# Kernel optimization log

Hardware: AMD Instinct MI355X
Metric: run time of the kernel (lower is better)

Reference implementation:

```python
import jax, jax.numpy as jnp
import numpy as np

B, S, D_IN, D_OUT = 4, 2048, 1024, 64
USE_MASK = True

def setup_inputs() -> dict:
    key = jax.random.key(0)
    ks = jax.random.split(key, 6)
    return {
        "inputs_for_keys": jax.random.normal(ks[0], (B, S, D_IN), jnp.float32),
        "inputs_for_values": jax.random.normal(ks[1], (B, S, D_IN), jnp.float32),
        "inputs_for_queries": jax.random.normal(ks[2], (B, S, D_IN), jnp.float32),
        "Weight_Q": jax.random.normal(ks[3], (D_IN, D_OUT), jnp.float32) * 0.02,
        "Weight_K": jax.random.normal(ks[4], (D_IN, D_OUT), jnp.float32) * 0.02,
        "Weight_V": jax.random.normal(ks[5], (D_IN, D_OUT), jnp.float32) * 0.02,
    }

def reference(inputs_for_keys, inputs_for_values, inputs_for_queries, Weight_Q, Weight_K, Weight_V):
    Q = jnp.einsum('bsd,de->bse', inputs_for_queries, Weight_Q)
    K = jnp.einsum('bsd,de->bse', inputs_for_keys, Weight_K)
    V = jnp.einsum('bsd,de->bse', inputs_for_values, Weight_V)
    # scores: [B, S_q, S_k], scaled by sqrt(d_out)
    scores = jnp.einsum('bqe,bke->bqk', Q, K) / np.sqrt(D_OUT).astype(np.float32)
    if USE_MASK:
        # -inf strictly above the diagonal (causal mask), matching
        # transpose(tril(ones*-inf, -1)) in the original.
        q_idx = jnp.arange(S)[:, None]
        k_idx = jnp.arange(S)[None, :]
        scores = jnp.where(k_idx > q_idx, -jnp.inf, scores)
    attn = jax.nn.softmax(scores, axis=-1)
    return jnp.einsum('bqk,bke->bqe', attn, V)
```

## Files before the change

### kernel.cpp

```cpp
#include <hip/hip_runtime.h>
#include <hip/hip_bf16.h>
#include <stdint.h>

typedef __bf16 bf16_t;
typedef __bf16 bf16x8 __attribute__((ext_vector_type(8)));
typedef float f32x4 __attribute__((ext_vector_type(4)));

#define L2E 1.44269504088896340736f

static __device__ __forceinline__ f32x4 mfma16(bf16x8 a, bf16x8 b, f32x4 c) {
  return __builtin_amdgcn_mfma_f32_16x16x32_bf16(a, b, c, 0, 0, 0);
}

static __device__ __forceinline__ void gload_lds16(const void* g, void* l) {
  __builtin_amdgcn_global_load_lds(
      (const __attribute__((address_space(1))) uint32_t*)g,
      (__attribute__((address_space(3))) uint32_t*)l, 16, 0, 0);
}

__global__ __launch_bounds__(256) void wt_kernel(const float* __restrict__ Wq,
                                                 const float* __restrict__ Wk,
                                                 const float* __restrict__ Wv,
                                                 bf16_t* __restrict__ Wt) {
  int gid = blockIdx.x * 256 + threadIdx.x;
  int proj = gid >> 16;
  int rem = gid & 65535;
  int k = rem >> 6, n = rem & 63;
  const float* W = (proj == 0) ? Wq : (proj == 1) ? Wk : Wv;
  float v = W[rem];
  if (proj == 0) v *= 0.125f;
  Wt[proj * 65536 + n * 1024 + k] = (bf16_t)v;
}

__global__ __launch_bounds__(384, 1) void proj_kernel(
    const float* __restrict__ Xq, const float* __restrict__ Xk, const float* __restrict__ Xv,
    const bf16_t* __restrict__ Wt,
    bf16_t* __restrict__ Qb, bf16_t* __restrict__ Kb, bf16_t* __restrict__ Vt) {
  __shared__ alignas(16) char Wl[131072];
  __shared__ alignas(16) bf16_t Osm[6][16][72];

  int tid = threadIdx.x;
  int w = tid / 64, lane = tid & 63;
  int l15 = lane & 15, g = lane >> 4;
  int bid = blockIdx.x;

  int p_lds = (bid * 6 + 2) >> 9;

  {
    const char* wb = (const char*)(Wt + (size_t)p_lds * 65536);
    for (int n = w; n < 64; n += 6) {
#pragma unroll
      for (int h = 0; h < 2; ++h) {
        const char* src = wb + n * 2048 + h * 1024 + ((lane * 16) ^ ((n & 7) << 4));
        gload_lds16(src, Wl + n * 2048 + h * 1024);
      }
    }
  }
  __syncthreads();

  int T = bid * 6 + w;
  int p = T >> 9;
  int t = T & 511;
  int m0 = t * 16;
  const float* X = (p == 0) ? Xq : (p == 1) ? Xk : Xv;
  const float* xrow = X + (size_t)(m0 + l15) * 1024 + g * 8;

  f32x4 acc[4] = {};

  auto wfrag_lds = [&](int ct, int byteoff) -> bf16x8 {
    int n = ct * 16 + l15;
    return *(const bf16x8*)(Wl + n * 2048 + (byteoff ^ ((n & 7) << 4)));
  };
  auto wfrag_glob = [&](int ct, int byteoff) -> bf16x8 {
    int n = ct * 16 + l15;
    return *(const bf16x8*)((const char*)(Wt + (size_t)p * 65536) + n * 2048 + byteoff);
  };

  auto run = [&](auto wf) {
    float4 pa[2][4];
    auto ld = [&](int j, float4* r) {
      const float* b = xrow + j * 64;
      r[0] = *(const float4*)b;        r[1] = *(const float4*)(b + 4);
      r[2] = *(const float4*)(b + 32); r[3] = *(const float4*)(b + 36);
    };
    ld(0, pa[0]);
#pragma unroll
    for (int j = 0; j < 16; ++j) {
      if (j < 15) ld(j + 1, pa[(j + 1) & 1]);
      float4* r = pa[j & 1];
      bf16x8 a0, a1;
      a0[0] = (bf16_t)r[0].x; a0[1] = (bf16_t)r[0].y; a0[2] = (bf16_t)r[0].z; a0[3] = (bf16_t)r[0].w;
      a0[4] = (bf16_t)r[1].x; a0[5] = (bf16_t)r[1].y; a0[6] = (bf16_t)r[1].z; a0[7] = (bf16_t)r[1].w;
      a1[0] = (bf16_t)r[2].x; a1[1] = (bf16_t)r[2].y; a1[2] = (bf16_t)r[2].z; a1[3] = (bf16_t)r[2].w;
      a1[4] = (bf16_t)r[3].x; a1[5] = (bf16_t)r[3].y; a1[6] = (bf16_t)r[3].z; a1[7] = (bf16_t)r[3].w;
#pragma unroll
      for (int ct = 0; ct < 4; ++ct) {
        acc[ct] = mfma16(a0, wf(ct, j * 128 + g * 16), acc[ct]);
        acc[ct] = mfma16(a1, wf(ct, j * 128 + 64 + g * 16), acc[ct]);
      }
    }
  };
  if (p == p_lds) run(wfrag_lds); else run(wfrag_glob);

#pragma unroll
  for (int ct = 0; ct < 4; ++ct)
#pragma unroll
    for (int r = 0; r < 4; ++r)
      Osm[w][g * 4 + r][ct * 16 + l15] = (bf16_t)acc[ct][r];

  if (p < 2) {
    bf16_t* Ob = (p == 0) ? Qb : Kb;
    int row = lane >> 2, c0 = (lane & 3) * 16;
    uint4 v0 = *(const uint4*)&Osm[w][row][c0];
    uint4 v1 = *(const uint4*)&Osm[w][row][c0 + 8];
    *(uint4*)&Ob[(size_t)(m0 + row) * 64 + c0] = v0;
    *(uint4*)&Ob[(size_t)(m0 + row) * 64 + c0 + 8] = v1;
  } else {
    int d = lane;
    bf16_t tmp[16];
#pragma unroll
    for (int s = 0; s < 16; ++s) tmp[s] = Osm[w][s][d];
    int b = t >> 7, s0 = (t & 127) * 16;
    bf16_t* dst = Vt + ((size_t)(b * 64 + d)) * 2048 + s0;
    *(uint4*)dst = *(const uint4*)&tmp[0];
    *(uint4*)(dst + 8) = *(const uint4*)&tmp[8];
  }
}

#define NW 8
__global__ __launch_bounds__(512) void attn_kernel(
    const bf16_t* __restrict__ Qb, const bf16_t* __restrict__ Kb,
    const bf16_t* __restrict__ Vt, float* __restrict__ Out) {
  __shared__ alignas(16) char Psm[NW * 4096];
  __shared__ float accL[NW][32][64];
  __shared__ float mL[NW][32];
  __shared__ float lL[NW][32];

  int b = blockIdx.y;
  int x = blockIdx.x;
  int qt = (b >= 2) ? (63 - x) : x;
  int q0 = qt * 32;
  int tid = threadIdx.x;
  int w = tid >> 6, lane = tid & 63;
  int l15 = lane & 15, g = lane >> 4;
  char* Pw = Psm + w * 4096;

  bf16x8 qf[2][2];
#pragma unroll
  for (int h = 0; h < 2; ++h) {
    size_t qrow = (size_t)(b * 2048 + q0 + h * 16 + l15) * 64;
    qf[h][0] = *(const bf16x8*)(Qb + qrow + g * 8);
    qf[h][1] = *(const bf16x8*)(Qb + qrow + 32 + g * 8);
  }

  float m_run[2][4], l_run[2][4];
  f32x4 acc_o[2][4] = {};
#pragma unroll
  for (int h = 0; h < 2; ++h)
#pragma unroll
    for (int r = 0; r < 4; ++r) { m_run[h][r] = -1e30f; l_run[h][r] = 0.f; }

  int ntiles = (q0 + 95) >> 6;
  const bf16_t* kbase = Kb + (size_t)b * 2048 * 64;
  const bf16_t* vbase = Vt + (size_t)b * 64 * 2048;

  for (int t = w; t < ntiles; t += NW) {
    int kv0 = t * 64;
    f32x4 s[2][4] = {};
#pragma unroll
    for (int ct = 0; ct < 4; ++ct) {
      const bf16_t* kr = kbase + (size_t)(kv0 + ct * 16 + l15) * 64 + g * 8;
      bf16x8 kf0 = *(const bf16x8*)kr;
      bf16x8 kf1 = *(const bf16x8*)(kr + 32);
#pragma unroll
      for (int h = 0; h < 2; ++h) {
        s[h][ct] = mfma16(qf[h][0], kf0, s[h][ct]);
        s[h][ct] = mfma16(qf[h][1], kf1, s[h][ct]);
      }
    }
    if (t == ntiles - 1) {
#pragma unroll
      for (int h = 0; h < 2; ++h)
#pragma unroll
        for (int ct = 0; ct < 4; ++ct)
#pragma unroll
          for (int r = 0; r < 4; ++r) {
            int kg_ = kv0 + ct * 16 + l15;
            int qg_ = q0 + h * 16 + g * 4 + r;
            if (kg_ > qg_) s[h][ct][r] = -1e30f;
          }
    }

#pragma unroll
    for (int h = 0; h < 2; ++h)
#pragma unroll
      for (int r = 0; r < 4; ++r) {
        float mx = fmaxf(fmaxf(s[h][0][r], s[h][1][r]), fmaxf(s[h][2][r], s[h][3][r]));
        mx = fmaxf(mx, __shfl_xor(mx, 1, 64));
        mx = fmaxf(mx, __shfl_xor(mx, 2, 64));
        mx = fmaxf(mx, __shfl_xor(mx, 4, 64));
        mx = fmaxf(mx, __shfl_xor(mx, 8, 64));
        float mnew = fmaxf(m_run[h][r], mx);
        float scale = exp2f((m_run[h][r] - mnew) * L2E);
        m_run[h][r] = mnew;
        float ps = 0.f;
        int qrl = h * 16 + g * 4 + r;
        char* pb = Pw + qrl * 128;
        int swp = (qrl & 7) << 4;
#pragma unroll
        for (int ct = 0; ct < 4; ++ct) {
          float p = exp2f((s[h][ct][r] - mnew) * L2E);
          ps += p;
          *(bf16_t*)(pb + ((ct * 32 + l15 * 2) ^ swp)) = (bf16_t)p;
        }
        ps += __shfl_xor(ps, 1, 64);
        ps += __shfl_xor(ps, 2, 64);
        ps += __shfl_xor(ps, 4, 64);
        ps += __shfl_xor(ps, 8, 64);
        l_run[h][r] = l_run[h][r] * scale + ps;
#pragma unroll
        for (int dt = 0; dt < 4; ++dt) acc_o[h][dt][r] *= scale;
      }

    int swpr = (l15 & 7) << 4;
#pragma unroll
    for (int ks = 0; ks < 2; ++ks) {
      bf16x8 pf0 = *(const bf16x8*)(Pw + l15 * 128 + ((ks * 64 + g * 16) ^ swpr));
      bf16x8 pf1 = *(const bf16x8*)(Pw + (16 + l15) * 128 + ((ks * 64 + g * 16) ^ swpr));
#pragma unroll
      for (int dt = 0; dt < 4; ++dt) {
        const bf16_t* vr = vbase + (size_t)(dt * 16 + l15) * 2048 + kv0 + ks * 32 + g * 8;
        bf16x8 vf = *(const bf16x8*)vr;
        acc_o[0][dt] = mfma16(pf0, vf, acc_o[0][dt]);
        acc_o[1][dt] = mfma16(pf1, vf, acc_o[1][dt]);
      }
    }
  }

  if (l15 == 0) {
#pragma unroll
    for (int h = 0; h < 2; ++h)
#pragma unroll
      for (int r = 0; r < 4; ++r) {
        mL[w][h * 16 + g * 4 + r] = m_run[h][r];
        lL[w][h * 16 + g * 4 + r] = l_run[h][r];
      }
  }
#pragma unroll
  for (int h = 0; h < 2; ++h)
#pragma unroll
    for (int dt = 0; dt < 4; ++dt)
#pragma unroll
      for (int r = 0; r < 4; ++r)
        accL[w][h * 16 + g * 4 + r][dt * 16 + l15] = acc_o[h][dt][r];
  __syncthreads();

  int row = tid >> 4, c0 = (tid & 15) * 4;
  float M = -1e30f;
#pragma unroll
  for (int w2 = 0; w2 < NW; ++w2) M = fmaxf(M, mL[w2][row]);
  float L = 0.f;
  f32x4 o = {0.f, 0.f, 0.f, 0.f};
#pragma unroll
  for (int w2 = 0; w2 < NW; ++w2) {
    float sc = exp2f((mL[w2][row] - M) * L2E);
    L += lL[w2][row] * sc;
    f32x4 a = *(const f32x4*)&accL[w2][row][c0];
    o[0] += sc * a[0]; o[1] += sc * a[1]; o[2] += sc * a[2]; o[3] += sc * a[3];
  }
  float inv = 1.0f / L;
  float4 o4 = {o[0] * inv, o[1] * inv, o[2] * inv, o[3] * inv};
  *(float4*)&Out[(size_t)(b * 2048 + q0 + row) * 64 + c0] = o4;
}

extern "C" void kernel_launch(void* const* d_in, const int* in_sizes, int n_in,
                              void* d_out, int out_size, void* d_ws, size_t ws_size,
                              hipStream_t stream) {
  const float* Xk = (const float*)d_in[0];
  const float* Xv = (const float*)d_in[1];
  const float* Xq = (const float*)d_in[2];
  const float* Wq = (const float*)d_in[3];
  const float* Wk = (const float*)d_in[4];
  const float* Wv = (const float*)d_in[5];
  float* Out = (float*)d_out;

  bf16_t* ws = (bf16_t*)d_ws;
  bf16_t* Qb = ws;
  bf16_t* Kb = ws + 524288;
  bf16_t* Vt = ws + 1048576;
  bf16_t* Wt = ws + 1572864;

  wt_kernel<<<dim3(768), dim3(256), 0, stream>>>(Wq, Wk, Wv, Wt);
  proj_kernel<<<dim3(256), dim3(384), 0, stream>>>(Xq, Xk, Xv, Wt, Qb, Kb, Vt);
  attn_kernel<<<dim3(64, 4), dim3(512), 0, stream>>>(Qb, Kb, Vt, Out);
}
```

Measured before the change: 54.05 us.

## Split fp32-to-bf16 input conversion into separate kernel before projection GEMM

Adds a standalone kernel that converts the three fp32 input activations to bf16 in workspace, and changes the projection GEMM to read bf16 rows with 16-byte loads, double-buffered in groups of eight fragments. This removes the per-element conversion from the GEMM's inner loop and halves the bytes the GEMM reads from X. In exchange it adds a full extra pass that reads 100MB of fp32 and writes 50MB of bf16, plus an additional kernel launch.

Result: slower. 72.61 us (+34.3%).

```diff
diff --git a/kernel.cpp b/kernel.cpp
--- a/kernel.cpp
+++ b/kernel.cpp
@@ -32,9 +32,24 @@
   Wt[proj * 65536 + n * 1024 + k] = (bf16_t)v;
 }
 
-__global__ __launch_bounds__(384, 1) void proj_kernel(
+__global__ __launch_bounds__(256) void convert_kernel(
     const float* __restrict__ Xq, const float* __restrict__ Xk, const float* __restrict__ Xv,
-    const bf16_t* __restrict__ Wt,
+    bf16_t* __restrict__ Xb) {
+  int p = blockIdx.y;
+  const float* X = (p == 0) ? Xq : (p == 1) ? Xk : Xv;
+  bf16_t* dst = Xb + (size_t)p * 8388608;
+  int tid = blockIdx.x * 256 + threadIdx.x;
+#pragma unroll 8
+  for (int i = 0; i < 8; ++i) {
+    size_t e = (size_t)(i * 262144 + tid) * 4;
+    float4 v = *(const float4*)(X + e);
+    bf16_t o4[4] = {(bf16_t)v.x, (bf16_t)v.y, (bf16_t)v.z, (bf16_t)v.w};
+    *(uint2*)(dst + e) = *(const uint2*)o4;
+  }
+}
+
+__global__ __launch_bounds__(384, 1) void gemm_kernel(
+    const bf16_t* __restrict__ Xb, const bf16_t* __restrict__ Wt,
     bf16_t* __restrict__ Qb, bf16_t* __restrict__ Kb, bf16_t* __restrict__ Vt) {
   __shared__ alignas(16) char Wl[131072];
   __shared__ alignas(16) bf16_t Osm[6][16][72];
@@ -62,8 +77,7 @@
   int p = T >> 9;
   int t = T & 511;
   int m0 = t * 16;
-  const float* X = (p == 0) ? Xq : (p == 1) ? Xk : Xv;
-  const float* xrow = X + (size_t)(m0 + l15) * 1024 + g * 8;
+  const bf16_t* xrow = Xb + (size_t)p * 8388608 + (size_t)(m0 + l15) * 1024 + g * 8;
 
   f32x4 acc[4] = {};
 
@@ -77,28 +91,29 @@
   };
 
   auto run = [&](auto wf) {
-    float4 pa[2][4];
-    auto ld = [&](int j, float4* r) {
-      const float* b = xrow + j * 64;
-      r[0] = *(const float4*)b;        r[1] = *(const float4*)(b + 4);
-      r[2] = *(const float4*)(b + 32); r[3] = *(const float4*)(b + 36);
+    bf16x8 A0[8], A1[8];
+    auto ldA = [&](int G, bf16x8* buf) {
+#pragma unroll
+      for (int i = 0; i < 8; ++i)
+        buf[i] = *(const bf16x8*)(xrow + (G * 8 + i) * 32);
     };
-    ld(0, pa[0]);
-#pragma unroll
-    for (int j = 0; j < 16; ++j) {
-      if (j < 15) ld(j + 1, pa[(j + 1) & 1]);
-      float4* r = pa[j & 1];
-      bf16x8 a0, a1;
-      a0[0] = (bf16_t)r[0].x; a0[1] = (bf16_t)r[0].y; a0[2] = (bf16_t)r[0].z; a0[3] = (bf16_t)r[0].w;
-      a0[4] = (bf16_t)r[1].x; a0[5] = (bf16_t)r[1].y; a0[6] = (bf16_t)r[1].z; a0[7] = (bf16_t)r[1].w;
-      a1[0] = (bf16_t)r[2].x; a1[1] = (bf16_t)r[2].y; a1[2] = (bf16_t)r[2].z; a1[3] = (bf16_t)r[2].w;
-      a1[4] = (bf16_t)r[3].x; a1[5] = (bf16_t)r[3].y; a1[6] = (bf16_t)r[3].z; a1[7] = (bf16_t)r[3].w;
-#pragma unroll
-      for (int ct = 0; ct < 4; ++ct) {
-        acc[ct] = mfma16(a0, wf(ct, j * 128 + g * 16), acc[ct]);
-        acc[ct] = mfma16(a1, wf(ct, j * 128 + 64 + g * 16), acc[ct]);
-      }
-    }
+    auto cmp = [&](int G, const bf16x8* buf) {
+#pragma unroll
+      for (int i = 0; i < 8; ++i) {
+        int j = G * 8 + i;
+#pragma unroll
+        for (int ct = 0; ct < 4; ++ct)
+          acc[ct] = mfma16(buf[i], wf(ct, j * 64 + g * 16), acc[ct]);
+      }
+    };
+    ldA(0, A0);
+    ldA(1, A1);
+    cmp(0, A0);
+    ldA(2, A0);
+    cmp(1, A1);
+    ldA(3, A1);
+    cmp(2, A0);
+    cmp(3, A1);
   };
   if (p == p_lds) run(wfrag_lds); else run(wfrag_glob);
 
@@ -289,8 +304,10 @@
   bf16_t* Kb = ws + 524288;
   bf16_t* Vt = ws + 1048576;
   bf16_t* Wt = ws + 1572864;
+  bf16_t* Xb = ws + 2097152;
 
   wt_kernel<<<dim3(768), dim3(256), 0, stream>>>(Wq, Wk, Wv, Wt);
-  proj_kernel<<<dim3(256), dim3(384), 0, stream>>>(Xq, Xk, Xv, Wt, Qb, Kb, Vt);
+  convert_kernel<<<dim3(1024, 3), dim3(256), 0, stream>>>(Xq, Xk, Xv, Xb);
+  gemm_kernel<<<dim3(256), dim3(384), 0, stream>>>(Xb, Wt, Qb, Kb, Vt);
   attn_kernel<<<dim3(64, 4), dim3(512), 0, stream>>>(Qb, Kb, Vt, Out);
 }
```
